# Optimization experiments

Hardware: AMD Instinct MI355X
Metric: run time of the kernel (lower is better)

Reference implementation:

```python
import jax, jax.numpy as jnp
import numpy as np
from jax import lax

TAGSET = 48
START_TAG = 46
STOP_TAG = 47
B, T = 128, 256

def setup_inputs() -> dict:
    key = jax.random.key(0)
    k1, k2, k3 = jax.random.split(key, 3)
    features = jax.random.normal(k1, (B, T, TAGSET, TAGSET), dtype=jnp.float32)
    targets = jax.random.randint(k2, (B, T), 0, TAGSET * TAGSET, dtype=jnp.int64)
    # lengths in [1, T], sorted descending as pack_padded_sequence expects
    lengths = jnp.sort(jax.random.randint(k3, (B,), 1, T + 1, dtype=jnp.int64))[::-1]
    return {"features": features, "targets": targets, "lengths": lengths}

def reference(features, targets, lengths):
    b, t, k, _ = features.shape
    # gold score: gather flattened (from_tag*K + to_tag) scores, sum over valid timesteps
    gathered = jnp.take_along_axis(
        features.reshape(b, t, k * k), targets[..., None], axis=2
    ).squeeze(-1)  # (B, T)
    valid = jnp.arange(t)[None, :] < lengths[:, None]  # (B, T) bool
    gold_score = jnp.sum(jnp.where(valid, gathered, 0.0))

    # forward algorithm: t=0 initializes from START_TAG row (all lengths >= 1)
    init = features[:, 0, START_TAG, :]  # (B, K)

    def step(scores_upto_t, inputs):
        feats_t, mask_t = inputs  # (B, K, K), (B,)
        upd = jax.nn.logsumexp(feats_t + scores_upto_t[:, :, None], axis=1)  # lse over from-tag
        new = jnp.where(mask_t[:, None], upd, scores_upto_t)  # freeze finished sequences
        return new, None

    feats_rest = jnp.swapaxes(features[:, 1:], 0, 1)  # (T-1, B, K, K)
    mask_rest = jnp.swapaxes(valid[:, 1:], 0, 1)      # (T-1, B)
    final, _ = lax.scan(step, init, (feats_rest, mask_rest))
    all_paths_scores = final[:, STOP_TAG].sum()
    return all_paths_scores - gold_score
```

## Files before the change

kernel.cpp:

```cpp
#include <hip/hip_runtime.h>


#define NB 128
#define NT 256
#define NK 48
#define NKK (NK * NK)
#define TAG_START 46
#define TAG_STOP 47

#define STEP_BARRIER() asm volatile("s_waitcnt lgkmcnt(0)\n\ts_barrier" ::: "memory")

#define LD12(v, p, ST) \
  v##0 = (p)[0*(ST)];  v##1 = (p)[1*(ST)];  v##2  = (p)[2*(ST)];  v##3  = (p)[3*(ST)]; \
  v##4 = (p)[4*(ST)];  v##5 = (p)[5*(ST)];  v##6  = (p)[6*(ST)];  v##7  = (p)[7*(ST)]; \
  v##8 = (p)[8*(ST)];  v##9 = (p)[9*(ST)];  v##10 = (p)[10*(ST)]; v##11 = (p)[11*(ST)];

#define STEPB(v, ST) { \
  const float* sc_ = &sv[(u + 1) & 1][rb]; \
  float4 s0 = *(const float4*)(sc_);     \
  float4 s1 = *(const float4*)(sc_ + 4); \
  float4 s2 = *(const float4*)(sc_ + 8); \
  if (((u - 1) & 3) == 0) { \
    float mm = fmaxf(fmaxf(fmaxf(s0.x,s0.y),fmaxf(s0.z,s0.w)), \
                     fmaxf(fmaxf(s1.x,s1.y),fmaxf(s1.z,s1.w))); \
    mm = fmaxf(mm, fmaxf(fmaxf(s2.x,s2.y),fmaxf(s2.z,s2.w))); \
    mm = fmaxf(mm, __shfl_xor(mm, 1, 64)); \
    mm = fmaxf(mm, __shfl_xor(mm, 2, 64)); \
    c += mm; \
    s0.x-=mm; s0.y-=mm; s0.z-=mm; s0.w-=mm; \
    s1.x-=mm; s1.y-=mm; s1.z-=mm; s1.w-=mm; \
    s2.x-=mm; s2.y-=mm; s2.z-=mm; s2.w-=mm; \
  } \
  float acc = (((__expf(v##0 + s0.x) + __expf(v##1 + s0.y)) + \
                (__expf(v##2 + s0.z) + __expf(v##3 + s0.w))) + \
               ((__expf(v##4 + s1.x) + __expf(v##5 + s1.y)) + \
                (__expf(v##6 + s1.z) + __expf(v##7 + s1.w)))) + \
              ((__expf(v##8 + s2.x) + __expf(v##9 + s2.y)) + \
               (__expf(v##10 + s2.z) + __expf(v##11 + s2.w))); \
  acc += __shfl_xor(acc, 1, 64); \
  acc += __shfl_xor(acc, 2, 64); \
  if (store) sv[u & 1][oo] = __logf(acc); \
  { int up_ = u + 2; if (up_ > nsteps) up_ = nsteps; \
    const float* p_ = basep + (long)up_ * dstep; LD12(v, p_, ST) } \
  STEP_BARRIER(); \
}

#define CHAIN(ST) { \
  float a0,a1,a2,a3,a4,a5,a6,a7,a8,a9,a10,a11; \
  float b0,b1,b2,b3,b4,b5,b6,b7,b8,b9,b10,b11; \
  { const float* p_ = basep + dstep; LD12(a, p_, ST) } \
  { int up_ = (2 > nsteps) ? nsteps : 2; \
    const float* p_ = basep + (long)up_ * dstep; LD12(b, p_, ST) } \
  __syncthreads(); \
  int u = 1; \
  for (;;) { \
    STEPB(a, ST) \
    if (++u > nsteps) break; \
    STEPB(b, ST) \
    if (++u > nsteps) break; \
  } \
}

__global__ __launch_bounds__(256, 1)
void viterbi_chain_kernel(const float* __restrict__ feats,
                          const int* __restrict__ targets,
                          const int* __restrict__ lengths,
                          float* __restrict__ out,
                          float* __restrict__ ws)
{
    const int bu  = blockIdx.x;
    const int b   = bu >> 1;
    const int dir = bu & 1;
    const int tid = threadIdx.x;
    const int len = lengths[b], last = len - 1, m = last >> 1;
    const float* __restrict__ fb = feats + (size_t)b * (NT * NKK);

    __shared__ float sv[2][NK];
    __shared__ float gred[4];

    {
        int tg  = dir ? (m + 1 + tid) : tid;
        int tmx = dir ? last : m;
        float g = 0.f;
        if (tg <= tmx) g = fb[(size_t)tg * NKK + targets[b * NT + tg]];
        #pragma unroll
        for (int o = 32; o; o >>= 1) g += __shfl_down(g, o, 64);
        if ((tid & 63) == 0) gred[tid >> 6] = g;
    }

    if (tid < NK) {
        float iv;
        if (dir) iv = (last == 0) ? ((tid == TAG_STOP) ? 0.f : -1e30f)
                                  : fb[(size_t)last * NKK + tid * NK + TAG_STOP];
        else     iv = fb[TAG_START * NK + tid];
        sv[0][tid] = iv;
    }

    const int lane = tid & 63, w = tid >> 6, qq = lane & 3, rb = qq * 12;
    const int oo   = w * 12 + (lane >> 2);
    const int ooc  = (oo < NK) ? oo : (NK - 1);
    const bool store = ((lane >> 2) < 12) && (qq == 0);

    int nsteps = dir ? (last - 1 - m) : m;
    if (nsteps < 0) nsteps = 0;

    float c = 0.f;
    if (nsteps > 0) {
        if (dir) {
            const float* basep = fb + (size_t)last * NKK + (size_t)ooc * NK + rb;
            const long dstep = -(long)NKK;
            CHAIN(1)
        } else {
            const float* basep = fb + (size_t)rb * NK + ooc;
            const long dstep = (long)NKK;
            CHAIN(NK)
        }
    } else {
        __syncthreads();
    }

    if (tid < NK) ws[(size_t)bu * 64 + tid] = sv[nsteps & 1][tid];
    if (tid == 0) {
        ws[(size_t)bu * 64 + 48] = c;
        atomicAdd(out, -(gred[0] + gred[1] + gred[2] + gred[3]));
    }
}

__global__ __launch_bounds__(64, 1)
void viterbi_combine_kernel(const float* __restrict__ ws,
                            float* __restrict__ out)
{
    const int b = blockIdx.x, lane = threadIdx.x;
    const float* f = ws + (size_t)(2 * b) * 64;
    const float* g = ws + (size_t)(2 * b + 1) * 64;
    float v = -3.0e38f;
    if (lane < NK) v = f[lane] + g[lane];
    float mm = v;
    #pragma unroll
    for (int o = 32; o; o >>= 1) mm = fmaxf(mm, __shfl_xor(mm, o, 64));
    float e = (lane < NK) ? __expf(v - mm) : 0.f;
    #pragma unroll
    for (int o = 32; o; o >>= 1) e += __shfl_xor(e, o, 64);
    if (lane == 0) atomicAdd(out, __logf(e) + mm + f[NK] + g[NK]);
}

extern "C" void kernel_launch(void* const* d_in, const int* in_sizes, int n_in,
                              void* d_out, int out_size, void* d_ws, size_t ws_size,
                              hipStream_t stream) {
    const float* feats   = (const float*)d_in[0];
    const int*   targets = (const int*)d_in[1];
    const int*   lengths = (const int*)d_in[2];
    float*       out     = (float*)d_out;
    float*       ws      = (float*)d_ws;

    hipMemsetAsync(out, 0, sizeof(float), stream);
    viterbi_chain_kernel<<<dim3(2 * NB), dim3(NT), 0, stream>>>(feats, targets, lengths, out, ws);
    viterbi_combine_kernel<<<dim3(NB), dim3(64), 0, stream>>>(ws, out);
}
```

Measured before the change: 409.6 us.

## Deepen feature prefetch to three steps and move barrier before shared reads

The kernel now keeps four rotating register sets of feature values, so loads are issued three steps ahead instead of two. It also issues those loads right after the shared-memory reads rather than after the store. The per-step barrier moves to the start of each step and yields a fake zero offset, which keeps the compiler from hoisting the shared reads above it. A final __syncthreads is added before the result write-back. The aim is to hide more global-load latency on the serial recurrence, at the cost of higher register pressure.

```diff
diff --git a/kernel.cpp b/kernel.cpp
--- a/kernel.cpp
+++ b/kernel.cpp
@@ -8,18 +8,22 @@
 #define TAG_START 46
 #define TAG_STOP 47
 
-#define STEP_BARRIER() asm volatile("s_waitcnt lgkmcnt(0)\n\ts_barrier" ::: "memory")
+#define BARRIER_DEF_ZERO(z) \
+  asm volatile("s_mov_b32 %0, 0\n\ts_waitcnt lgkmcnt(0)\n\ts_barrier" : "=s"(z))
 
 #define LD12(v, p, ST) \
   v##0 = (p)[0*(ST)];  v##1 = (p)[1*(ST)];  v##2  = (p)[2*(ST)];  v##3  = (p)[3*(ST)]; \
   v##4 = (p)[4*(ST)];  v##5 = (p)[5*(ST)];  v##6  = (p)[6*(ST)];  v##7  = (p)[7*(ST)]; \
   v##8 = (p)[8*(ST)];  v##9 = (p)[9*(ST)];  v##10 = (p)[10*(ST)]; v##11 = (p)[11*(ST)];
 
-#define STEPB(v, ST) { \
-  const float* sc_ = &sv[(u + 1) & 1][rb]; \
+#define STEPB(cur, nxt, ST) { \
+  int z_; BARRIER_DEF_ZERO(z_); \
+  const float* sc_ = &sv[(u + 1) & 1][rb] + z_; \
   float4 s0 = *(const float4*)(sc_);     \
   float4 s1 = *(const float4*)(sc_ + 4); \
   float4 s2 = *(const float4*)(sc_ + 8); \
+  { int up_ = u + 3; if (up_ > nsteps) up_ = nsteps; \
+    const float* p_ = basep + (long)up_ * dstep; LD12(nxt, p_, ST) } \
   if (((u - 1) & 3) == 0) { \
     float mm = fmaxf(fmaxf(fmaxf(s0.x,s0.y),fmaxf(s0.z,s0.w)), \
                      fmaxf(fmaxf(s1.x,s1.y),fmaxf(s1.z,s1.w))); \
@@ -31,33 +35,34 @@
     s1.x-=mm; s1.y-=mm; s1.z-=mm; s1.w-=mm; \
     s2.x-=mm; s2.y-=mm; s2.z-=mm; s2.w-=mm; \
   } \
-  float acc = (((__expf(v##0 + s0.x) + __expf(v##1 + s0.y)) + \
-                (__expf(v##2 + s0.z) + __expf(v##3 + s0.w))) + \
-               ((__expf(v##4 + s1.x) + __expf(v##5 + s1.y)) + \
-                (__expf(v##6 + s1.z) + __expf(v##7 + s1.w)))) + \
-              ((__expf(v##8 + s2.x) + __expf(v##9 + s2.y)) + \
-               (__expf(v##10 + s2.z) + __expf(v##11 + s2.w))); \
+  float acc = (((__expf(cur##0 + s0.x) + __expf(cur##1 + s0.y)) + \
+                (__expf(cur##2 + s0.z) + __expf(cur##3 + s0.w))) + \
+               ((__expf(cur##4 + s1.x) + __expf(cur##5 + s1.y)) + \
+                (__expf(cur##6 + s1.z) + __expf(cur##7 + s1.w)))) + \
+              ((__expf(cur##8 + s2.x) + __expf(cur##9 + s2.y)) + \
+               (__expf(cur##10 + s2.z) + __expf(cur##11 + s2.w))); \
   acc += __shfl_xor(acc, 1, 64); \
   acc += __shfl_xor(acc, 2, 64); \
-  if (store) sv[u & 1][oo] = __logf(acc); \
-  { int up_ = u + 2; if (up_ > nsteps) up_ = nsteps; \
-    const float* p_ = basep + (long)up_ * dstep; LD12(v, p_, ST) } \
-  STEP_BARRIER(); \
+  if (store) *(volatile float*)&sv[u & 1][oo] = __logf(acc); \
 }
 
 #define CHAIN(ST) { \
   float a0,a1,a2,a3,a4,a5,a6,a7,a8,a9,a10,a11; \
   float b0,b1,b2,b3,b4,b5,b6,b7,b8,b9,b10,b11; \
+  float c0,c1,c2,c3,c4,c5,c6,c7,c8,c9,c10,c11; \
+  float d0,d1,d2,d3,d4,d5,d6,d7,d8,d9,d10,d11; \
   { const float* p_ = basep + dstep; LD12(a, p_, ST) } \
-  { int up_ = (2 > nsteps) ? nsteps : 2; \
-    const float* p_ = basep + (long)up_ * dstep; LD12(b, p_, ST) } \
+  { int u_ = (2 > nsteps) ? nsteps : 2; \
+    const float* p_ = basep + (long)u_ * dstep; LD12(b, p_, ST) } \
+  { int u_ = (3 > nsteps) ? nsteps : 3; \
+    const float* p_ = basep + (long)u_ * dstep; LD12(c, p_, ST) } \
   __syncthreads(); \
   int u = 1; \
   for (;;) { \
-    STEPB(a, ST) \
-    if (++u > nsteps) break; \
-    STEPB(b, ST) \
-    if (++u > nsteps) break; \
+    STEPB(a, d, ST) if (++u > nsteps) break; \
+    STEPB(b, a, ST) if (++u > nsteps) break; \
+    STEPB(c, b, ST) if (++u > nsteps) break; \
+    STEPB(d, c, ST) if (++u > nsteps) break; \
   } \
 }
 
@@ -119,6 +124,8 @@
         __syncthreads();
     }
 
+    __syncthreads();
+
     if (tid < NK) ws[(size_t)bu * 64 + tid] = sv[nsteps & 1][tid];
     if (tid == 0) {
         ws[(size_t)bu * 64 + 48] = c;
```

New measurement: 446.0 us. 1.09x slower.
